# Performance work log

Hardware: AMD Instinct MI355X
Metric: run time of the kernel (lower is better)

## Reference

```python
import jax, jax.numpy as jnp
import numpy as np

# model dims
D = 2048      # hidden_size
H = 16        # num_attention_heads
KV = 4        # num_key_value_heads
DH = 128      # head_dim
RD = 64       # rotary_dim (partial RoPE)
E = 8         # num_local_experts
TOPK = 2      # num_experts_per_tok
I = 1024      # intermediate_size
EPS = 1e-6
THETA = 1000000.0


def rmsnorm(h, w, eps=EPS):
    dt = h.dtype
    h32 = h.astype(jnp.float32)
    var = jnp.mean(h32 * h32, axis=-1, keepdims=True)
    return (w * (h32 * jax.lax.rsqrt(var + eps))).astype(dt)


def rotate_half(t):
    half = t.shape[-1] // 2
    return jnp.concatenate([-t[..., half:], t[..., :half]], axis=-1)


def setup_inputs() -> dict:
    key = jax.random.key(0)
    ks = jax.random.split(key, 16)
    s = lambda k, shape, sc: (jax.random.normal(k, shape, dtype=jnp.float32) * sc)
    B, S = 1, 2048
    return {
        "x": s(ks[0], (B, S, D), 1.0),
        "ln1_w": jnp.ones((D,), jnp.float32),
        "ln2_w": jnp.ones((D,), jnp.float32),
        "wq": s(ks[1], (D, H * DH), 0.02),
        "wk": s(ks[2], (D, KV * DH), 0.02),
        "wv": s(ks[3], (D, KV * DH), 0.02),
        "wo": s(ks[4], (H * DH, D), 0.02),
        "qnorm_w": jnp.ones((H * DH,), jnp.float32),
        "knorm_w": jnp.ones((KV * DH,), jnp.float32),
        "router_w": s(ks[5], (D, E), 0.02),
        "router_bias": s(ks[6], (E,), 0.1),
        "wg": s(ks[7], (E, D, I), 0.02),
        "wu": s(ks[8], (E, D, I), 0.02),
        "wd": s(ks[9], (E, I, D), 0.02),
    }


def reference(x, ln1_w, ln2_w, wq, wk, wv, wo, qnorm_w, knorm_w,
              router_w, router_bias, wg, wu, wd):
    B, S, _ = x.shape
    # ---- input RMSNorm + attention ----
    res = x
    h = rmsnorm(x, ln1_w)
    q = h @ wq                           # [B,S,H*DH]
    k = h @ wk                           # [B,S,KV*DH]
    v = h @ wv
    # MiniMax M2: QK-norm BEFORE reshape, over the full projection dim
    q = rmsnorm(q, qnorm_w)
    k = rmsnorm(k, knorm_w)
    q = q.reshape(B, S, H, DH).transpose(0, 2, 1, 3)    # [B,H,S,DH]
    k = k.reshape(B, S, KV, DH).transpose(0, 2, 1, 3)   # [B,KV,S,DH]
    v = v.reshape(B, S, KV, DH).transpose(0, 2, 1, 3)
    # partial RoPE on first RD dims of each head
    pos = jnp.arange(S, dtype=jnp.float32)
    inv_freq = 1.0 / (THETA ** (jnp.arange(0, RD, 2, dtype=jnp.float32) / RD))
    ang = pos[:, None] * inv_freq[None, :]              # [S,RD/2]
    emb = jnp.concatenate([ang, ang], axis=-1)          # [S,RD]
    cos, sin = jnp.cos(emb), jnp.sin(emb)

    def rope(t):
        rot, pas = t[..., :RD], t[..., RD:]
        rot = rot * cos + rotate_half(rot) * sin
        return jnp.concatenate([rot, pas], axis=-1)

    q, k = rope(q), rope(k)
    # GQA: repeat kv heads
    rep = H // KV
    k = jnp.repeat(k, rep, axis=1)                      # [B,H,S,DH]
    v = jnp.repeat(v, rep, axis=1)
    scores = jnp.einsum("bhqd,bhkd->bhqk", q, k) / np.sqrt(DH)
    causal = jnp.tril(jnp.ones((S, S), dtype=bool))
    scores = jnp.where(causal, scores, jnp.finfo(jnp.float32).min)
    attn = jax.nn.softmax(scores.astype(jnp.float32), axis=-1).astype(q.dtype)
    o = jnp.einsum("bhqk,bhkd->bhqd", attn, v)          # [B,H,S,DH]
    o = o.transpose(0, 2, 1, 3).reshape(B, S, H * DH) @ wo
    x1 = res + o

    # ---- post-attn RMSNorm + sigmoid-router top-k MoE ----
    h2 = rmsnorm(x1, ln2_w)
    t = h2.reshape(-1, D)                               # [T,D]
    T = t.shape[0]
    logits = t.astype(jnp.float32) @ router_w           # router in fp32
    sig = jax.nn.sigmoid(logits)                        # act before topk
    # bias only influences expert choice, not affinities
    _, topi = jax.lax.top_k(sig + router_bias, TOPK)    # [T,TOPK]
    aff = jnp.take_along_axis(sig, topi, axis=-1)
    aff = aff / jnp.sum(aff, axis=-1, keepdims=True)    # normalize_top_k_affinities
    combine = jnp.zeros((T, E), jnp.float32).at[
        jnp.arange(T)[:, None], topi].set(aff)          # [T,E] sparse combine weights
    # GLU expert MLPs (dense over experts; combine zeros out unrouted)
    gate = jnp.einsum("td,edi->tei", t, wg)
    up = jnp.einsum("td,edi->tei", t, wu)
    act = jax.nn.silu(gate) * up                        # [T,E,I]
    moe = jnp.einsum("te,tei,eid->td", combine.astype(t.dtype), act, wd)
    return x1 + moe.reshape(B, S, D)
```

## Files before the change

### kernel.cpp

```cpp
#include <hip/hip_runtime.h>
#include <hip/hip_bf16.h>
#include <stdint.h>
#include <math.h>

typedef __bf16 bf16;
typedef __bf16 bf16x8 __attribute__((ext_vector_type(8)));
typedef __bf16 bf16x4 __attribute__((ext_vector_type(4)));
typedef float  f32x4  __attribute__((ext_vector_type(4)));

#define SD 2048
#define DM 2048
#define NH 16
#define NKV 4
#define DHD 128
#define NE 8
#define NNI 1024

constexpr size_t OF_WQKVT = 0;
constexpr size_t OF_WGUT  = OF_WQKVT + 12582912ull;
constexpr size_t OF_WDT   = OF_WGUT  + 67108864ull;
constexpr size_t OF_WOT   = OF_WDT   + 33554432ull;
constexpr size_t OF_H     = OF_WOT   + 8388608ull;
constexpr size_t OF_QKV   = OF_H     + 8388608ull;
constexpr size_t OF_QB    = OF_QKV   + 25165824ull;
constexpr size_t OF_KB    = OF_QB    + 8388608ull;
constexpr size_t OF_VTB   = OF_KB    + 2097152ull;
constexpr size_t OF_X1    = OF_VTB   + 2097152ull;
constexpr size_t WS_NEED  = OF_X1    + 16777216ull;
constexpr size_t OF_ACT  = OF_QKV;
constexpr size_t OF_TB   = OF_WOT;
constexpr size_t OF_OB   = OF_H;
constexpr size_t OF_CNT  = OF_KB;
constexpr size_t OF_BLKE = OF_KB + 256;
constexpr size_t OF_BLKR = OF_KB + 512;
constexpr size_t OF_TOT  = OF_KB + 768;
constexpr size_t OF_TOPI = OF_KB + 1024;
constexpr size_t OF_TOPW = OF_KB + 16384;
constexpr size_t OF_IDXL = OF_KB + 65536;
constexpr size_t OF_WLST = OF_KB + 131072;
constexpr size_t OF_TMP0 = OF_H;
constexpr size_t OF_TMP1 = OF_WOT;

__device__ __forceinline__ void async16(void* lds, const void* g) {
  uint32_t lo = (uint32_t)(uintptr_t)lds;
  __builtin_amdgcn_global_load_lds(
      (const __attribute__((address_space(1))) uint32_t*)(uintptr_t)g,
      (__attribute__((address_space(3))) uint32_t*)lo,
      16, 0, 0);
}

__global__ void transpose_cvt(const float* __restrict__ in, int ild, long long inb,
                              bf16* __restrict__ out, int old_, long long outb,
                              int ost, int oroff)
{
  __shared__ float tile[32][33];
  const float* ip = in + (long long)blockIdx.z * inb;
  bf16* op = out + (long long)blockIdx.z * outb;
  int r0 = blockIdx.y * 32, c0 = blockIdx.x * 32;
  int tx = threadIdx.x, ty = threadIdx.y;
#pragma unroll
  for (int i = 0; i < 4; i++)
    tile[ty + i*8][tx] = ip[(size_t)(r0 + ty + i*8)*ild + c0 + tx];
  __syncthreads();
#pragma unroll
  for (int i = 0; i < 4; i++) {
    int cl = ty + i*8;
    op[(size_t)((c0 + cl)*ost + oroff)*old_ + r0 + tx] = (bf16)tile[tx][cl];
  }
}

__global__ __launch_bounds__(256)
void rmsnorm_k(const float* __restrict__ in, const float* __restrict__ w, bf16* __restrict__ outb)
{
  __shared__ float red[4];
  int s = blockIdx.x, t = threadIdx.x;
  const float* ip = in + (size_t)s * DM;
  float v[8]; float ss = 0.f;
#pragma unroll
  for (int i = 0; i < 8; i++) { v[i] = ip[t + i*256]; ss += v[i]*v[i]; }
#pragma unroll
  for (int off = 32; off > 0; off >>= 1) ss += __shfl_xor(ss, off);
  if ((t & 63) == 0) red[t >> 6] = ss;
  __syncthreads();
  float rn = rsqrtf((red[0]+red[1]+red[2]+red[3]) * (1.f/DM) + 1e-6f);
  bf16* op = outb + (size_t)s * DM;
#pragma unroll
  for (int i = 0; i < 8; i++) op[t + i*256] = (bf16)(v[i]*rn*w[t + i*256]);
}

__global__ __launch_bounds__(256)
void qrope_k(const float* __restrict__ qkv, const float* __restrict__ w, bf16* __restrict__ qout)
{
  __shared__ float row[2048];
  __shared__ float red[4];
  int s = blockIdx.x, t = threadIdx.x;
  const float* ip = qkv + (size_t)s * 3072;
  float ss = 0.f;
#pragma unroll
  for (int i = 0; i < 8; i++) { float x = ip[t + i*256]; row[t + i*256] = x; ss += x*x; }
#pragma unroll
  for (int off = 32; off > 0; off >>= 1) ss += __shfl_xor(ss, off);
  if ((t & 63) == 0) red[t >> 6] = ss;
  __syncthreads();
  float rn = rsqrtf((red[0]+red[1]+red[2]+red[3]) * (1.f/2048.f) + 1e-6f);
  const float sc = 0.08838834764831845f;
#pragma unroll
  for (int i = 0; i < 8; i++) {
    int idx = t + i*256;
    int d = idx & 127;
    float val = row[idx]*rn*w[idx];
    float o;
    if (d < 64) {
      int fi = d & 31;
      float ang = (float)s * expf(-(float)fi * (13.815510557964274f/32.f));
      float c, sn; sincosf(ang, &sn, &c);
      float pv = row[idx ^ 32]*rn*w[idx ^ 32];
      o = (d < 32) ? (val*c - pv*sn) : (val*c + pv*sn);
    } else o = val;
    qout[((size_t)(idx >> 7)*SD + s)*DHD + d] = (bf16)(o * sc);
  }
}

__global__ __launch_bounds__(128)
void krope_k(const float* __restrict__ qkv, const float* __restrict__ w, bf16* __restrict__ kout)
{
  __shared__ float row[512];
  __shared__ float red[2];
  int s = blockIdx.x, t = threadIdx.x;
  const float* ip = qkv + (size_t)s * 3072 + 2048;
  float ss = 0.f;
#pragma unroll
  for (int i = 0; i < 4; i++) { float x = ip[t + i*128]; row[t + i*128] = x; ss += x*x; }
#pragma unroll
  for (int off = 32; off > 0; off >>= 1) ss += __shfl_xor(ss, off);
  if ((t & 63) == 0) red[t >> 6] = ss;
  __syncthreads();
  float rn = rsqrtf((red[0]+red[1]) * (1.f/512.f) + 1e-6f);
#pragma unroll
  for (int i = 0; i < 4; i++) {
    int idx = t + i*128;
    int d = idx & 127;
    float val = row[idx]*rn*w[idx];
    float o;
    if (d < 64) {
      int fi = d & 31;
      float ang = (float)s * expf(-(float)fi * (13.815510557964274f/32.f));
      float c, sn; sincosf(ang, &sn, &c);
      float pv = row[idx ^ 32]*rn*w[idx ^ 32];
      o = (d < 32) ? (val*c - pv*sn) : (val*c + pv*sn);
    } else o = val;
    kout[((size_t)(idx >> 7)*SD + s)*DHD + d] = (bf16)o;
  }
}

template<int EPI>
__global__ __launch_bounds__(256)
void gemm_bt(const bf16* __restrict__ Ag, const bf16* __restrict__ Bg,
             float* __restrict__ Cg, const float* __restrict__ res,
             int M, int N, int K)
{
  __shared__ __align__(16) bf16 As[2][128*32];
  __shared__ __align__(16) bf16 Bs[2][128*32];
  const int tid = threadIdx.x;
  const int wv = tid >> 6, l = tid & 63;
  const int wm = wv >> 1, wn = wv & 1;
  const int bm = blockIdx.y * 128, bn = blockIdx.x * 128;
  const bf16* A  = Ag;
  const bf16* BT = Bg;

  f32x4 acc[4][4];
  const f32x4 vz = {0.f, 0.f, 0.f, 0.f};
#pragma unroll
  for (int i = 0; i < 4; i++)
#pragma unroll
    for (int j = 0; j < 4; j++) acc[i][j] = vz;

  auto stage = [&](int kt, int b) {
    int k0 = kt * 32;
#pragma unroll
    for (int c = 0; c < 2; c++) {
      int chunk = wv*2 + c;
      int row = chunk*16 + (l >> 2);
      int kc = (l & 3) * 8;
      async16(&As[b][chunk*512], A  + (size_t)(bm + row)*K + k0 + kc);
      async16(&Bs[b][chunk*512], BT + (size_t)(bn + row)*K + k0 + kc);
    }
  };

  int nkt = K >> 5;
  stage(0, 0);
  int buf = 0;
  for (int kt = 0; kt < nkt; ++kt) {
    __syncthreads();
    if (kt + 1 < nkt) stage(kt + 1, buf ^ 1);
    bf16x8 af[4], bfv[4];
#pragma unroll
    for (int m = 0; m < 4; m++)
      af[m] = *(const bf16x8*)&As[buf][(wm*64 + m*16 + (l & 15))*32 + (l >> 4)*8];
#pragma unroll
    for (int n = 0; n < 4; n++)
      bfv[n] = *(const bf16x8*)&Bs[buf][(wn*64 + n*16 + (l & 15))*32 + (l >> 4)*8];
#pragma unroll
    for (int m = 0; m < 4; m++)
#pragma unroll
      for (int n = 0; n < 4; n++)
        acc[m][n] = __builtin_amdgcn_mfma_f32_16x16x32_bf16(af[m], bfv[n], acc[m][n], 0, 0, 0);
    buf ^= 1;
  }

#pragma unroll
  for (int m = 0; m < 4; m++) {
#pragma unroll
    for (int n = 0; n < 4; n++) {
#pragma unroll
      for (int r = 0; r < 4; r++) {
        int row = bm + wm*64 + m*16 + (l >> 4)*4 + r;
        int col = bn + wn*64 + n*16 + (l & 15);
        float v = acc[m][n][r];
        if (EPI == 0) {
          Cg[(size_t)row*N + col] = v;
        } else {
          Cg[(size_t)row*N + col] = v + res[(size_t)row*N + col];
        }
      }
    }
  }
}

__global__ __launch_bounds__(256)
void gemm_moe_gu(const bf16* __restrict__ tb, const bf16* __restrict__ wgu,
                 bf16* __restrict__ act,
                 const int* __restrict__ cnt, const int* __restrict__ blk_e,
                 const int* __restrict__ blk_r0, const int* __restrict__ total_nblk,
                 const int* __restrict__ idxlist)
{
  const int by = blockIdx.y;
  if (by >= *total_nblk) return;
  const int e = blk_e[by], r0 = blk_r0[by], cn = cnt[e];
  __shared__ __align__(16) bf16 As[2][128*32];
  __shared__ __align__(16) bf16 Bs[2][128*32];
  const int tid = threadIdx.x;
  const int wv = tid >> 6, l = tid & 63;
  const int wm = wv >> 1, wn = wv & 1;
  const int bn = blockIdx.x * 128;
  const bf16* BT = wgu + (size_t)e*2048*2048;

  const bf16* Arow[2];
#pragma unroll
  for (int c = 0; c < 2; c++) {
    int chunk = wv*2 + c;
    int rp = r0 + chunk*16 + (l >> 2);
    int tok = (rp < cn) ? (idxlist[e*2048 + rp] & 0xFFFF) : 0;
    Arow[c] = tb + (size_t)tok*2048 + (l & 3)*8;
  }

  f32x4 acc[4][4];
  const f32x4 vz = {0.f, 0.f, 0.f, 0.f};
#pragma unroll
  for (int i = 0; i < 4; i++)
#pragma unroll
    for (int j = 0; j < 4; j++) acc[i][j] = vz;

  auto stage = [&](int kt, int b) {
    int k0 = kt * 32;
#pragma unroll
    for (int c = 0; c < 2; c++) {
      int chunk = wv*2 + c;
      int row = chunk*16 + (l >> 2);
      int kc = (l & 3) * 8;
      async16(&As[b][chunk*512], Arow[c] + k0);
      async16(&Bs[b][chunk*512], BT + (size_t)(bn + row)*2048 + k0 + kc);
    }
  };

  stage(0, 0);
  int buf = 0;
  for (int kt = 0; kt < 64; ++kt) {
    __syncthreads();
    if (kt + 1 < 64) stage(kt + 1, buf ^ 1);
    bf16x8 af[4], bfv[4];
#pragma unroll
    for (int m = 0; m < 4; m++)
      af[m] = *(const bf16x8*)&As[buf][(wm*64 + m*16 + (l & 15))*32 + (l >> 4)*8];
#pragma unroll
    for (int n = 0; n < 4; n++)
      bfv[n] = *(const bf16x8*)&Bs[buf][(wn*64 + n*16 + (l & 15))*32 + (l >> 4)*8];
#pragma unroll
    for (int m = 0; m < 4; m++)
#pragma unroll
      for (int n = 0; n < 4; n++)
        acc[m][n] = __builtin_amdgcn_mfma_f32_16x16x32_bf16(af[m], bfv[n], acc[m][n], 0, 0, 0);
    buf ^= 1;
  }

  bf16* ap = act + (size_t)e*2048*1024;
#pragma unroll
  for (int m = 0; m < 4; m++) {
#pragma unroll
    for (int n = 0; n < 4; n++) {
#pragma unroll
      for (int r = 0; r < 4; r++) {
        int lrow = wm*64 + m*16 + (l >> 4)*4 + r;
        int col = bn + wn*64 + n*16 + (l & 15);
        float v = acc[m][n][r];
        float p = __shfl_xor(v, 1);
        if (!(l & 1)) {
          float a = v / (1.f + __expf(-v)) * p;
          ap[(size_t)(r0 + lrow)*1024 + (col >> 1)] = (bf16)a;
        }
      }
    }
  }
}

__global__ __launch_bounds__(256)
void gemm_moe_dn(const bf16* __restrict__ act, const bf16* __restrict__ wdt,
                 bf16* __restrict__ tmp0, bf16* __restrict__ tmp1,
                 const int* __restrict__ cnt, const int* __restrict__ blk_e,
                 const int* __restrict__ blk_r0, const int* __restrict__ total_nblk,
                 const int* __restrict__ idxlist, const float* __restrict__ wlist)
{
  const int by = blockIdx.y;
  if (by >= *total_nblk) return;
  const int e = blk_e[by], r0 = blk_r0[by], cn = cnt[e];
  __shared__ __align__(16) bf16 As[2][128*32];
  __shared__ __align__(16) bf16 Bs[2][128*32];
  const int tid = threadIdx.x;
  const int wv = tid >> 6, l = tid & 63;
  const int wm = wv >> 1, wn = wv & 1;
  const int bn = blockIdx.x * 128;
  const bf16* A  = act + (size_t)e*2048*1024 + (size_t)r0*1024;
  const bf16* BT = wdt + (size_t)e*2048*1024;

  f32x4 acc[4][4];
  const f32x4 vz = {0.f, 0.f, 0.f, 0.f};
#pragma unroll
  for (int i = 0; i < 4; i++)
#pragma unroll
    for (int j = 0; j < 4; j++) acc[i][j] = vz;

  auto stage = [&](int kt, int b) {
    int k0 = kt * 32;
#pragma unroll
    for (int c = 0; c < 2; c++) {
      int chunk = wv*2 + c;
      int row = chunk*16 + (l >> 2);
      int kc = (l & 3) * 8;
      async16(&As[b][chunk*512], A  + (size_t)row*1024 + k0 + kc);
      async16(&Bs[b][chunk*512], BT + (size_t)(bn + row)*1024 + k0 + kc);
    }
  };

  stage(0, 0);
  int buf = 0;
  for (int kt = 0; kt < 32; ++kt) {
    __syncthreads();
    if (kt + 1 < 32) stage(kt + 1, buf ^ 1);
    bf16x8 af[4], bfv[4];
#pragma unroll
    for (int m = 0; m < 4; m++)
      af[m] = *(const bf16x8*)&As[buf][(wm*64 + m*16 + (l & 15))*32 + (l >> 4)*8];
#pragma unroll
    for (int n = 0; n < 4; n++)
      bfv[n] = *(const bf16x8*)&Bs[buf][(wn*64 + n*16 + (l & 15))*32 + (l >> 4)*8];
#pragma unroll
    for (int m = 0; m < 4; m++)
#pragma unroll
      for (int n = 0; n < 4; n++)
        acc[m][n] = __builtin_amdgcn_mfma_f32_16x16x32_bf16(af[m], bfv[n], acc[m][n], 0, 0, 0);
    buf ^= 1;
  }

#pragma unroll
  for (int m = 0; m < 4; m++) {
#pragma unroll
    for (int n = 0; n < 4; n++) {
#pragma unroll
      for (int r = 0; r < 4; r++) {
        int lrow = wm*64 + m*16 + (l >> 4)*4 + r;
        int rie = r0 + lrow;
        if (rie < cn) {
          int col = bn + wn*64 + n*16 + (l & 15);
          int pk = idxlist[e*2048 + rie];
          int t = pk & 0xFFFF, rank = pk >> 16;
          float w = wlist[e*2048 + rie];
          bf16* dst = rank ? tmp1 : tmp0;
          dst[(size_t)t*2048 + col] = (bf16)(w * acc[m][n][r]);
        }
      }
    }
  }
}

__global__ __launch_bounds__(256)
void router_k(const float* __restrict__ x1, const float* __restrict__ w2,
              const float* __restrict__ rw, const float* __restrict__ rb,
              int* __restrict__ top_i, float* __restrict__ top_w)
{
  int tok = blockIdx.x*4 + (threadIdx.x >> 6);
  int l = threadIdx.x & 63;
  const float* ip = x1 + (size_t)tok * DM;
  float tv[32]; float ss = 0.f;
#pragma unroll
  for (int i = 0; i < 32; i++) { float v = ip[l + i*64]; tv[i] = v; ss += v*v; }
#pragma unroll
  for (int off = 32; off > 0; off >>= 1) ss += __shfl_xor(ss, off);
  float rn = rsqrtf(ss * (1.f/DM) + 1e-6f);
  float acc[8];
#pragma unroll
  for (int e = 0; e < 8; e++) acc[e] = 0.f;
#pragma unroll
  for (int i = 0; i < 32; i++) {
    int d = l + i*64;
    float tval = tv[i]*rn*w2[d];
#pragma unroll
    for (int e = 0; e < 8; e++) acc[e] += tval * rw[d*8 + e];
  }
#pragma unroll
  for (int e = 0; e < 8; e++)
#pragma unroll
    for (int off = 32; off > 0; off >>= 1) acc[e] += __shfl_xor(acc[e], off);
  if (l == 0) {
    float sig[8], scv[8];
#pragma unroll
    for (int e = 0; e < 8; e++) { sig[e] = 1.f/(1.f + expf(-acc[e])); scv[e] = sig[e] + rb[e]; }
    int i0 = 0;
#pragma unroll
    for (int e = 1; e < 8; e++) if (scv[e] > scv[i0]) i0 = e;
    int i1 = (i0 == 0) ? 1 : 0;
#pragma unroll
    for (int e = 0; e < 8; e++) if (e != i0 && scv[e] > scv[i1]) i1 = e;
    float a0 = sig[i0], a1 = sig[i1], inv = 1.f/(a0 + a1);
    top_i[tok] = i0 | (i1 << 8);
    top_w[tok*2]   = a0*inv;
    top_w[tok*2+1] = a1*inv;
  }
}

__global__ __launch_bounds__(256)
void build_k(const int* __restrict__ top_i, const float* __restrict__ top_w,
             int* __restrict__ cnt, int* __restrict__ blk_e, int* __restrict__ blk_r0,
             int* __restrict__ total_nblk, int* __restrict__ idxlist, float* __restrict__ wlist)
{
  __shared__ int lcnt[8];
  int tid = threadIdx.x;
  if (tid < 8) lcnt[tid] = 0;
  __syncthreads();
  for (int t = tid; t < SD; t += 256) {
    int pk = top_i[t];
    int i0 = pk & 0xFF, i1 = (pk >> 8) & 0xFF;
    int p0 = atomicAdd(&lcnt[i0], 1);
    idxlist[i0*2048 + p0] = t;
    wlist [i0*2048 + p0] = top_w[t*2];
    int p1 = atomicAdd(&lcnt[i1], 1);
    idxlist[i1*2048 + p1] = t | (1 << 16);
    wlist [i1*2048 + p1] = top_w[t*2+1];
  }
  __syncthreads();
  if (tid < 8) cnt[tid] = lcnt[tid];
  if (tid == 0) {
    int tot = 0;
    for (int e = 0; e < 8; e++) {
      int nb = (lcnt[e] + 127) >> 7;
      for (int b = 0; b < nb; b++) { blk_e[tot] = e; blk_r0[tot] = b*128; tot++; }
    }
    *total_nblk = tot;
  }
}

__global__ __launch_bounds__(256)
void final_add(const float* __restrict__ x1, const bf16* __restrict__ t0,
               const bf16* __restrict__ t1, float* __restrict__ out)
{
  size_t i = ((size_t)blockIdx.x*256 + threadIdx.x) * 4;
  f32x4 a = *(const f32x4*)(x1 + i);
  bf16x4 b0 = *(const bf16x4*)(t0 + i);
  bf16x4 b1 = *(const bf16x4*)(t1 + i);
  f32x4 o;
#pragma unroll
  for (int j = 0; j < 4; j++) o[j] = a[j] + (float)b0[j] + (float)b1[j];
  *(f32x4*)(out + i) = o;
}

__global__ __launch_bounds__(256)
void flash(const bf16* __restrict__ qb, const bf16* __restrict__ kb,
           const bf16* __restrict__ vtb, bf16* __restrict__ ob)
{
  __shared__ __align__(16) bf16 Ks[64*128];
  __shared__ __align__(16) bf16 Vs[128*64];
  __shared__ __align__(16) bf16 Ps[4*16*64];
  const int tid = threadIdx.x, wv = tid >> 6, l = tid & 63;
  const int qt = blockIdx.x, h = blockIdx.y, g = h >> 2;

  const int qrow = qt*64 + wv*16 + (l & 15);
  bf16x8 qf[4];
#pragma unroll
  for (int f = 0; f < 4; f++)
    qf[f] = *(const bf16x8*)(qb + ((size_t)h*SD + qrow)*DHD + f*32 + (l >> 4)*8);

  float mrun[4], lrun[4];
#pragma unroll
  for (int r = 0; r < 4; r++) { mrun[r] = -1e30f; lrun[r] = 0.f; }
  f32x4 oac[8];
  const f32x4 vz = {0.f, 0.f, 0.f, 0.f};
#pragma unroll
  for (int d = 0; d < 8; d++) oac[d] = vz;

  for (int j = 0; j <= qt; ++j) {
#pragma unroll
    for (int c = 0; c < 4; c++) {
      int chunk = wv*4 + c;
      int rk = chunk*4 + (l >> 4);
      int ck = (l & 15) ^ (rk & 7);
      async16(&Ks[chunk*512], kb + ((size_t)g*SD + j*64 + rk)*DHD + ck*8);
      int rv = chunk*8 + (l >> 3);
      int cv = (l & 7) ^ (rv & 7);
      async16(&Vs[chunk*512], vtb + ((size_t)g*DHD + rv)*SD + j*64 + cv*8);
    }
    __syncthreads();

    f32x4 sf[4];
#pragma unroll
    for (int n = 0; n < 4; n++) sf[n] = vz;
#pragma unroll
    for (int f = 0; f < 4; f++) {
#pragma unroll
      for (int n = 0; n < 4; n++) {
        int row = n*16 + (l & 15);
        int cb = (f*64 + (l >> 4)*16) ^ ((row & 7) << 4);
        bf16x8 kf = *(const bf16x8*)((const char*)Ks + row*256 + cb);
        sf[n] = __builtin_amdgcn_mfma_f32_16x16x32_bf16(qf[f], kf, sf[n], 0, 0, 0);
      }
    }
    if (j == qt) {
#pragma unroll
      for (int n = 0; n < 4; n++)
#pragma unroll
        for (int r = 0; r < 4; r++) {
          int kvp = n*16 + (l & 15);
          int qp  = wv*16 + (l >> 4)*4 + r;
          if (kvp > qp) sf[n][r] = -1e30f;
        }
    }
#pragma unroll
    for (int r = 0; r < 4; r++) {
      float tm = fmaxf(fmaxf(sf[0][r], sf[1][r]), fmaxf(sf[2][r], sf[3][r]));
#pragma unroll
      for (int off = 8; off > 0; off >>= 1) tm = fmaxf(tm, __shfl_xor(tm, off));
      float mn = fmaxf(mrun[r], tm);
      float fac = __expf(mrun[r] - mn);
      mrun[r] = mn;
      float pe[4]; float ps = 0.f;
#pragma unroll
      for (int n = 0; n < 4; n++) { pe[n] = __expf(sf[n][r] - mn); ps += pe[n]; }
#pragma unroll
      for (int off = 8; off > 0; off >>= 1) ps += __shfl_xor(ps, off);
      lrun[r] = lrun[r]*fac + ps;
#pragma unroll
      for (int d = 0; d < 8; d++) oac[d][r] *= fac;
      int prow = (l >> 4)*4 + r;
#pragma unroll
      for (int n = 0; n < 4; n++) {
        int cbp = ((n*16 + (l & 15))*2) ^ ((prow & 7) << 4);
        *(bf16*)((char*)Ps + wv*2048 + prow*128 + cbp) = (bf16)pe[n];
      }
    }
#pragma unroll
    for (int ks = 0; ks < 2; ks++) {
      int pr = l & 15;
      int cbp = (ks*64 + (l >> 4)*16) ^ ((pr & 7) << 4);
      bf16x8 pa = *(const bf16x8*)((const char*)Ps + wv*2048 + pr*128 + cbp);
#pragma unroll
      for (int dt = 0; dt < 8; dt++) {
        int rv = dt*16 + (l & 15);
        int cbv = (ks*64 + (l >> 4)*16) ^ ((rv & 7) << 4);
        bf16x8 vf = *(const bf16x8*)((const char*)Vs + rv*128 + cbv);
        oac[dt] = __builtin_amdgcn_mfma_f32_16x16x32_bf16(pa, vf, oac[dt], 0, 0, 0);
      }
    }
    __syncthreads();
  }
#pragma unroll
  for (int dt = 0; dt < 8; dt++)
#pragma unroll
    for (int r = 0; r < 4; r++) {
      int s = qt*64 + wv*16 + (l >> 4)*4 + r;
      int d = dt*16 + (l & 15);
      ob[(size_t)s*DM + h*DHD + d] = (bf16)(oac[dt][r] / lrun[r]);
    }
}

extern "C" void kernel_launch(void* const* d_in, const int* in_sizes, int n_in,
                              void* d_out, int out_size, void* d_ws, size_t ws_size,
                              hipStream_t stream) {
  if (ws_size < WS_NEED) return;
  const float* x     = (const float*)d_in[0];
  const float* ln1_w = (const float*)d_in[1];
  const float* ln2_w = (const float*)d_in[2];
  const float* wq    = (const float*)d_in[3];
  const float* wk    = (const float*)d_in[4];
  const float* wv    = (const float*)d_in[5];
  const float* wo    = (const float*)d_in[6];
  const float* qnw   = (const float*)d_in[7];
  const float* knw   = (const float*)d_in[8];
  const float* rw    = (const float*)d_in[9];
  const float* rb    = (const float*)d_in[10];
  const float* wg    = (const float*)d_in[11];
  const float* wu    = (const float*)d_in[12];
  const float* wd    = (const float*)d_in[13];

  char* ws = (char*)d_ws;
  bf16*  wqkvT = (bf16*)(ws + OF_WQKVT);
  bf16*  wguT  = (bf16*)(ws + OF_WGUT);
  bf16*  wdT   = (bf16*)(ws + OF_WDT);
  bf16*  woT   = (bf16*)(ws + OF_WOT);
  bf16*  hb    = (bf16*)(ws + OF_H);
  float* qkvf  = (float*)(ws + OF_QKV);
  bf16*  qbb   = (bf16*)(ws + OF_QB);
  bf16*  kbb   = (bf16*)(ws + OF_KB);
  bf16*  vtbb  = (bf16*)(ws + OF_VTB);
  float* x1f   = (float*)(ws + OF_X1);
  bf16*  actb  = (bf16*)(ws + OF_ACT);
  bf16*  tbb   = (bf16*)(ws + OF_TB);
  bf16*  obb   = (bf16*)(ws + OF_OB);
  int*   cntp  = (int*)(ws + OF_CNT);
  int*   blke  = (int*)(ws + OF_BLKE);
  int*   blkr  = (int*)(ws + OF_BLKR);
  int*   totp  = (int*)(ws + OF_TOT);
  int*   topi  = (int*)(ws + OF_TOPI);
  float* topw  = (float*)(ws + OF_TOPW);
  int*   idxl  = (int*)(ws + OF_IDXL);
  float* wlst  = (float*)(ws + OF_WLST);
  bf16*  tmp0  = (bf16*)(ws + OF_TMP0);
  bf16*  tmp1  = (bf16*)(ws + OF_TMP1);
  float* outp  = (float*)d_out;

  dim3 b32(32, 8);
  transpose_cvt<<<dim3(64,64,1), b32, 0, stream>>>(wq, 2048, 0, wqkvT, 2048, 0, 1, 0);
  transpose_cvt<<<dim3(16,64,1), b32, 0, stream>>>(wk,  512, 0, wqkvT, 2048, 0, 1, 2048);
  transpose_cvt<<<dim3(16,64,1), b32, 0, stream>>>(wv,  512, 0, wqkvT, 2048, 0, 1, 2560);
  transpose_cvt<<<dim3(64,64,1), b32, 0, stream>>>(wo, 2048, 0, woT,   2048, 0, 1, 0);
  transpose_cvt<<<dim3(32,64,8), b32, 0, stream>>>(wg, 1024, 2048ll*1024, wguT, 2048, 2048ll*2048, 2, 0);
  transpose_cvt<<<dim3(32,64,8), b32, 0, stream>>>(wu, 1024, 2048ll*1024, wguT, 2048, 2048ll*2048, 2, 1);
  transpose_cvt<<<dim3(64,32,8), b32, 0, stream>>>(wd, 2048, 1024ll*2048, wdT,  1024, 2048ll*1024, 1, 0);

  rmsnorm_k<<<2048, 256, 0, stream>>>(x, ln1_w, hb);
  gemm_bt<0><<<dim3(24,16,1), 256, 0, stream>>>(hb, wqkvT, qkvf, nullptr, 2048, 3072, 2048);
  qrope_k<<<2048, 256, 0, stream>>>(qkvf, qnw, qbb);
  krope_k<<<2048, 128, 0, stream>>>(qkvf, knw, kbb);
  transpose_cvt<<<dim3(16,64,1), b32, 0, stream>>>(qkvf + 2560, 3072, 0, vtbb, 2048, 0, 1, 0);

  flash<<<dim3(32,16,1), 256, 0, stream>>>(qbb, kbb, vtbb, obb);

  gemm_bt<1><<<dim3(16,16,1), 256, 0, stream>>>(obb, woT, x1f, x, 2048, 2048, 2048);
  rmsnorm_k<<<2048, 256, 0, stream>>>(x1f, ln2_w, tbb);
  router_k<<<512, 256, 0, stream>>>(x1f, ln2_w, rw, rb, topi, topw);
  build_k<<<1, 256, 0, stream>>>(topi, topw, cntp, blke, blkr, totp, idxl, wlst);

  gemm_moe_gu<<<dim3(16,40,1), 256, 0, stream>>>(tbb, wguT, actb, cntp, blke, blkr, totp, idxl);
  gemm_moe_dn<<<dim3(16,40,1), 256, 0, stream>>>(actb, wdT, tmp0, tmp1, cntp, blke, blkr, totp, idxl, wlst);
  final_add<<<4096, 256, 0, stream>>>(x1f, tmp0, tmp1, outp);
}
```

Before: 630.4 us.

## Shrink GEMM M-tiles to 64, double-buffer flash KV, precompute RoPE table

```diff
diff --git a/kernel.cpp b/kernel.cpp
--- a/kernel.cpp
+++ b/kernel.cpp
@@ -30,11 +30,12 @@
 constexpr size_t OF_ACT  = OF_QKV;
 constexpr size_t OF_TB   = OF_WOT;
 constexpr size_t OF_OB   = OF_H;
+constexpr size_t OF_ROPET= OF_X1;
 constexpr size_t OF_CNT  = OF_KB;
-constexpr size_t OF_BLKE = OF_KB + 256;
-constexpr size_t OF_BLKR = OF_KB + 512;
-constexpr size_t OF_TOT  = OF_KB + 768;
-constexpr size_t OF_TOPI = OF_KB + 1024;
+constexpr size_t OF_BLKE = OF_KB + 512;
+constexpr size_t OF_BLKR = OF_KB + 1024;
+constexpr size_t OF_TOT  = OF_KB + 1536;
+constexpr size_t OF_TOPI = OF_KB + 2048;
 constexpr size_t OF_TOPW = OF_KB + 16384;
 constexpr size_t OF_IDXL = OF_KB + 65536;
 constexpr size_t OF_WLST = OF_KB + 131072;
@@ -70,6 +71,17 @@
 }
 
 __global__ __launch_bounds__(256)
+void rope_tab_k(float* __restrict__ tab)
+{
+  int i = blockIdx.x*256 + threadIdx.x;
+  int s = i >> 5, fi = i & 31;
+  float ang = (float)s * expf(-(float)fi * (13.815510557964274f/32.f));
+  float c, sn; sincosf(ang, &sn, &c);
+  tab[i*2]   = c;
+  tab[i*2+1] = sn;
+}
+
+__global__ __launch_bounds__(256)
 void rmsnorm_k(const float* __restrict__ in, const float* __restrict__ w, bf16* __restrict__ outb)
 {
   __shared__ float red[4];
@@ -89,12 +101,14 @@
 }
 
 __global__ __launch_bounds__(256)
-void qrope_k(const float* __restrict__ qkv, const float* __restrict__ w, bf16* __restrict__ qout)
+void qrope_k(const float* __restrict__ qkv, const float* __restrict__ w,
+             const float* __restrict__ tab, bf16* __restrict__ qout)
 {
   __shared__ float row[2048];
   __shared__ float red[4];
   int s = blockIdx.x, t = threadIdx.x;
   const float* ip = qkv + (size_t)s * 3072;
+  const float2* tab2 = (const float2*)tab;
   float ss = 0.f;
 #pragma unroll
   for (int i = 0; i < 8; i++) { float x = ip[t + i*256]; row[t + i*256] = x; ss += x*x; }
@@ -112,22 +126,23 @@
     float o;
     if (d < 64) {
       int fi = d & 31;
-      float ang = (float)s * expf(-(float)fi * (13.815510557964274f/32.f));
-      float c, sn; sincosf(ang, &sn, &c);
+      float2 cs = tab2[s*32 + fi];
       float pv = row[idx ^ 32]*rn*w[idx ^ 32];
-      o = (d < 32) ? (val*c - pv*sn) : (val*c + pv*sn);
+      o = (d < 32) ? (val*cs.x - pv*cs.y) : (val*cs.x + pv*cs.y);
     } else o = val;
     qout[((size_t)(idx >> 7)*SD + s)*DHD + d] = (bf16)(o * sc);
   }
 }
 
 __global__ __launch_bounds__(128)
-void krope_k(const float* __restrict__ qkv, const float* __restrict__ w, bf16* __restrict__ kout)
+void krope_k(const float* __restrict__ qkv, const float* __restrict__ w,
+             const float* __restrict__ tab, bf16* __restrict__ kout)
 {
   __shared__ float row[512];
   __shared__ float red[2];
   int s = blockIdx.x, t = threadIdx.x;
   const float* ip = qkv + (size_t)s * 3072 + 2048;
+  const float2* tab2 = (const float2*)tab;
   float ss = 0.f;
 #pragma unroll
   for (int i = 0; i < 4; i++) { float x = ip[t + i*128]; row[t + i*128] = x; ss += x*x; }
@@ -144,46 +159,51 @@
     float o;
     if (d < 64) {
       int fi = d & 31;
-      float ang = (float)s * expf(-(float)fi * (13.815510557964274f/32.f));
-      float c, sn; sincosf(ang, &sn, &c);
+      float2 cs = tab2[s*32 + fi];
       float pv = row[idx ^ 32]*rn*w[idx ^ 32];
-      o = (d < 32) ? (val*c - pv*sn) : (val*c + pv*sn);
+      o = (d < 32) ? (val*cs.x - pv*cs.y) : (val*cs.x + pv*cs.y);
     } else o = val;
     kout[((size_t)(idx >> 7)*SD + s)*DHD + d] = (bf16)o;
   }
 }
 
-template<int EPI>
+template<int EPI, int BM>
 __global__ __launch_bounds__(256)
 void gemm_bt(const bf16* __restrict__ Ag, const bf16* __restrict__ Bg,
              float* __restrict__ Cg, const float* __restrict__ res,
              int M, int N, int K)
 {
-  __shared__ __align__(16) bf16 As[2][128*32];
+  constexpr int WM  = BM/2;
+  constexpr int MI  = WM/16;
+  constexpr int NCH = (BM+128)/16;
+  constexpr int CPW = NCH/4;
+  __shared__ __align__(16) bf16 As[2][BM*32];
   __shared__ __align__(16) bf16 Bs[2][128*32];
   const int tid = threadIdx.x;
   const int wv = tid >> 6, l = tid & 63;
   const int wm = wv >> 1, wn = wv & 1;
-  const int bm = blockIdx.y * 128, bn = blockIdx.x * 128;
+  const int bm = blockIdx.y * BM, bn = blockIdx.x * 128;
   const bf16* A  = Ag;
   const bf16* BT = Bg;
 
-  f32x4 acc[4][4];
+  f32x4 acc[MI][4];
   const f32x4 vz = {0.f, 0.f, 0.f, 0.f};
 #pragma unroll
-  for (int i = 0; i < 4; i++)
+  for (int i = 0; i < MI; i++)
 #pragma unroll
     for (int j = 0; j < 4; j++) acc[i][j] = vz;
 
   auto stage = [&](int kt, int b) {
     int k0 = kt * 32;
-#pragma unroll
-    for (int c = 0; c < 2; c++) {
-      int chunk = wv*2 + c;
+    int kc = (l & 3) * 8;
+#pragma unroll
+    for (int c = 0; c < CPW; c++) {
+      int chunk = wv*CPW + c;
       int row = chunk*16 + (l >> 2);
-      int kc = (l & 3) * 8;
-      async16(&As[b][chunk*512], A  + (size_t)(bm + row)*K + k0 + kc);
-      async16(&Bs[b][chunk*512], BT + (size_t)(bn + row)*K + k0 + kc);
+      if (chunk < BM/16)
+        async16(&As[b][chunk*512], A  + (size_t)(bm + row)*K + k0 + kc);
+      else
+        async16(&Bs[b][(chunk - BM/16)*512], BT + (size_t)(bn + row - BM)*K + k0 + kc);
     }
   };
 
@@ -193,15 +213,15 @@
   for (int kt = 0; kt < nkt; ++kt) {
     __syncthreads();
     if (kt + 1 < nkt) stage(kt + 1, buf ^ 1);
-    bf16x8 af[4], bfv[4];
-#pragma unroll
-    for (int m = 0; m < 4; m++)
-      af[m] = *(const bf16x8*)&As[buf][(wm*64 + m*16 + (l & 15))*32 + (l >> 4)*8];
+    bf16x8 af[MI], bfv[4];
+#pragma unroll
+    for (int m = 0; m < MI; m++)
+      af[m] = *(const bf16x8*)&As[buf][(wm*WM + m*16 + (l & 15))*32 + (l >> 4)*8];
 #pragma unroll
     for (int n = 0; n < 4; n++)
       bfv[n] = *(const bf16x8*)&Bs[buf][(wn*64 + n*16 + (l & 15))*32 + (l >> 4)*8];
 #pragma unroll
-    for (int m = 0; m < 4; m++)
+    for (int m = 0; m < MI; m++)
 #pragma unroll
       for (int n = 0; n < 4; n++)
         acc[m][n] = __builtin_amdgcn_mfma_f32_16x16x32_bf16(af[m], bfv[n], acc[m][n], 0, 0, 0);
@@ -209,12 +229,12 @@
   }
 
 #pragma unroll
-  for (int m = 0; m < 4; m++) {
+  for (int m = 0; m < MI; m++) {
 #pragma unroll
     for (int n = 0; n < 4; n++) {
 #pragma unroll
       for (int r = 0; r < 4; r++) {
-        int row = bm + wm*64 + m*16 + (l >> 4)*4 + r;
+        int row = bm + wm*WM + m*16 + (l >> 4)*4 + r;
         int col = bn + wn*64 + n*16 + (l & 15);
         float v = acc[m][n][r];
         if (EPI == 0) {
@@ -237,7 +257,7 @@
   const int by = blockIdx.y;
   if (by >= *total_nblk) return;
   const int e = blk_e[by], r0 = blk_r0[by], cn = cnt[e];
-  __shared__ __align__(16) bf16 As[2][128*32];
+  __shared__ __align__(16) bf16 As[2][64*32];
   __shared__ __align__(16) bf16 Bs[2][128*32];
   const int tid = threadIdx.x;
   const int wv = tid >> 6, l = tid & 63;
@@ -245,31 +265,37 @@
   const int bn = blockIdx.x * 128;
   const bf16* BT = wgu + (size_t)e*2048*2048;
 
-  const bf16* Arow[2];
-#pragma unroll
-  for (int c = 0; c < 2; c++) {
-    int chunk = wv*2 + c;
-    int rp = r0 + chunk*16 + (l >> 2);
-    int tok = (rp < cn) ? (idxlist[e*2048 + rp] & 0xFFFF) : 0;
-    Arow[c] = tb + (size_t)tok*2048 + (l & 3)*8;
-  }
-
-  f32x4 acc[4][4];
+  const bf16* Aptr[3];
+#pragma unroll
+  for (int c = 0; c < 3; c++) {
+    int chunk = wv*3 + c;
+    Aptr[c] = tb;
+    if (chunk < 4) {
+      int rp = r0 + chunk*16 + (l >> 2);
+      int tok = (rp < cn) ? (idxlist[e*2048 + rp] & 0xFFFF) : 0;
+      Aptr[c] = tb + (size_t)tok*2048 + (l & 3)*8;
+    }
+  }
+
+  f32x4 acc[2][4];
   const f32x4 vz = {0.f, 0.f, 0.f, 0.f};
 #pragma unroll
-  for (int i = 0; i < 4; i++)
+  for (int i = 0; i < 2; i++)
 #pragma unroll
     for (int j = 0; j < 4; j++) acc[i][j] = vz;
 
   auto stage = [&](int kt, int b) {
     int k0 = kt * 32;
-#pragma unroll
-    for (int c = 0; c < 2; c++) {
-      int chunk = wv*2 + c;
-      int row = chunk*16 + (l >> 2);
-      int kc = (l & 3) * 8;
-      async16(&As[b][chunk*512], Arow[c] + k0);
-      async16(&Bs[b][chunk*512], BT + (size_t)(bn + row)*2048 + k0 + kc);
+    int kc = (l & 3) * 8;
+#pragma unroll
+    for (int c = 0; c < 3; c++) {
+      int chunk = wv*3 + c;
+      if (chunk < 4)
+        async16(&As[b][chunk*512], Aptr[c] + k0);
+      else {
+        int row = chunk*16 + (l >> 2) - 64;
+        async16(&Bs[b][(chunk-4)*512], BT + (size_t)(bn + row)*2048 + k0 + kc);
+      }
     }
   };
 
@@ -278,15 +304,15 @@
   for (int kt = 0; kt < 64; ++kt) {
     __syncthreads();
     if (kt + 1 < 64) stage(kt + 1, buf ^ 1);
-    bf16x8 af[4], bfv[4];
-#pragma unroll
-    for (int m = 0; m < 4; m++)
-      af[m] = *(const bf16x8*)&As[buf][(wm*64 + m*16 + (l & 15))*32 + (l >> 4)*8];
+    bf16x8 af[2], bfv[4];
+#pragma unroll
+    for (int m = 0; m < 2; m++)
+      af[m] = *(const bf16x8*)&As[buf][(wm*32 + m*16 + (l & 15))*32 + (l >> 4)*8];
 #pragma unroll
     for (int n = 0; n < 4; n++)
       bfv[n] = *(const bf16x8*)&Bs[buf][(wn*64 + n*16 + (l & 15))*32 + (l >> 4)*8];
 #pragma unroll
-    for (int m = 0; m < 4; m++)
+    for (int m = 0; m < 2; m++)
 #pragma unroll
       for (int n = 0; n < 4; n++)
         acc[m][n] = __builtin_amdgcn_mfma_f32_16x16x32_bf16(af[m], bfv[n], acc[m][n], 0, 0, 0);
@@ -295,12 +321,12 @@
 
   bf16* ap = act + (size_t)e*2048*1024;
 #pragma unroll
-  for (int m = 0; m < 4; m++) {
+  for (int m = 0; m < 2; m++) {
 #pragma unroll
     for (int n = 0; n < 4; n++) {
 #pragma unroll
       for (int r = 0; r < 4; r++) {
-        int lrow = wm*64 + m*16 + (l >> 4)*4 + r;
+        int lrow = wm*32 + m*16 + (l >> 4)*4 + r;
         int col = bn + wn*64 + n*16 + (l & 15);
         float v = acc[m][n][r];
         float p = __shfl_xor(v, 1);
@@ -323,7 +349,7 @@
   const int by = blockIdx.y;
   if (by >= *total_nblk) return;
   const int e = blk_e[by], r0 = blk_r0[by], cn = cnt[e];
-  __shared__ __align__(16) bf16 As[2][128*32];
+  __shared__ __align__(16) bf16 As[2][64*32];
   __shared__ __align__(16) bf16 Bs[2][128*32];
   const int tid = threadIdx.x;
   const int wv = tid >> 6, l = tid & 63;
@@ -332,22 +358,24 @@
   const bf16* A  = act + (size_t)e*2048*1024 + (size_t)r0*1024;
   const bf16* BT = wdt + (size_t)e*2048*1024;
 
-  f32x4 acc[4][4];
+  f32x4 acc[2][4];
   const f32x4 vz = {0.f, 0.f, 0.f, 0.f};
 #pragma unroll
-  for (int i = 0; i < 4; i++)
+  for (int i = 0; i < 2; i++)
 #pragma unroll
     for (int j = 0; j < 4; j++) acc[i][j] = vz;
 
   auto stage = [&](int kt, int b) {
     int k0 = kt * 32;
-#pragma unroll
-    for (int c = 0; c < 2; c++) {
-      int chunk = wv*2 + c;
+    int kc = (l & 3) * 8;
+#pragma unroll
+    for (int c = 0; c < 3; c++) {
+      int chunk = wv*3 + c;
       int row = chunk*16 + (l >> 2);
-      int kc = (l & 3) * 8;
-      async16(&As[b][chunk*512], A  + (size_t)row*1024 + k0 + kc);
-      async16(&Bs[b][chunk*512], BT + (size_t)(bn + row)*1024 + k0 + kc);
+      if (chunk < 4)
+        async16(&As[b][chunk*512], A  + (size_t)row*1024 + k0 + kc);
+      else
+        async16(&Bs[b][(chunk-4)*512], BT + (size_t)(bn + row - 64)*1024 + k0 + kc);
     }
   };
 
@@ -356,15 +384,15 @@
   for (int kt = 0; kt < 32; ++kt) {
     __syncthreads();
     if (kt + 1 < 32) stage(kt + 1, buf ^ 1);
-    bf16x8 af[4], bfv[4];
-#pragma unroll
-    for (int m = 0; m < 4; m++)
-      af[m] = *(const bf16x8*)&As[buf][(wm*64 + m*16 + (l & 15))*32 + (l >> 4)*8];
+    bf16x8 af[2], bfv[4];
+#pragma unroll
+    for (int m = 0; m < 2; m++)
+      af[m] = *(const bf16x8*)&As[buf][(wm*32 + m*16 + (l & 15))*32 + (l >> 4)*8];
 #pragma unroll
     for (int n = 0; n < 4; n++)
       bfv[n] = *(const bf16x8*)&Bs[buf][(wn*64 + n*16 + (l & 15))*32 + (l >> 4)*8];
 #pragma unroll
-    for (int m = 0; m < 4; m++)
+    for (int m = 0; m < 2; m++)
 #pragma unroll
       for (int n = 0; n < 4; n++)
         acc[m][n] = __builtin_amdgcn_mfma_f32_16x16x32_bf16(af[m], bfv[n], acc[m][n], 0, 0, 0);
@@ -372,12 +400,12 @@
   }
 
 #pragma unroll
-  for (int m = 0; m < 4; m++) {
+  for (int m = 0; m < 2; m++) {
 #pragma unroll
     for (int n = 0; n < 4; n++) {
 #pragma unroll
       for (int r = 0; r < 4; r++) {
-        int lrow = wm*64 + m*16 + (l >> 4)*4 + r;
+        int lrow = wm*32 + m*16 + (l >> 4)*4 + r;
         int rie = r0 + lrow;
         if (rie < cn) {
           int col = bn + wn*64 + n*16 + (l & 15);
@@ -461,8 +489,8 @@
   if (tid == 0) {
     int tot = 0;
     for (int e = 0; e < 8; e++) {
-      int nb = (lcnt[e] + 127) >> 7;
-      for (int b = 0; b < nb; b++) { blk_e[tot] = e; blk_r0[tot] = b*128; tot++; }
+      int nb = (lcnt[e] + 63) >> 6;
+      for (int b = 0; b < nb; b++) { blk_e[tot] = e; blk_r0[tot] = b*64; tot++; }
     }
     *total_nblk = tot;
   }
@@ -486,11 +514,12 @@
 void flash(const bf16* __restrict__ qb, const bf16* __restrict__ kb,
            const bf16* __restrict__ vtb, bf16* __restrict__ ob)
 {
-  __shared__ __align__(16) bf16 Ks[64*128];
-  __shared__ __align__(16) bf16 Vs[128*64];
+  __shared__ __align__(16) bf16 Ks[2][64*128];
+  __shared__ __align__(16) bf16 Vs[2][128*64];
   __shared__ __align__(16) bf16 Ps[4*16*64];
   const int tid = threadIdx.x, wv = tid >> 6, l = tid & 63;
-  const int qt = blockIdx.x, h = blockIdx.y, g = h >> 2;
+  const int h = blockIdx.y, g = h >> 2;
+  const int qt = (h & 8) ? (31 - (int)blockIdx.x) : (int)blockIdx.x;
 
   const int qrow = qt*64 + wv*16 + (l & 15);
   bf16x8 qf[4];
@@ -506,32 +535,40 @@
 #pragma unroll
   for (int d = 0; d < 8; d++) oac[d] = vz;
 
-  for (int j = 0; j <= qt; ++j) {
+  auto stage = [&](int j, int b) {
 #pragma unroll
     for (int c = 0; c < 4; c++) {
       int chunk = wv*4 + c;
       int rk = chunk*4 + (l >> 4);
       int ck = (l & 15) ^ (rk & 7);
-      async16(&Ks[chunk*512], kb + ((size_t)g*SD + j*64 + rk)*DHD + ck*8);
+      async16(&Ks[b][chunk*512], kb + ((size_t)g*SD + j*64 + rk)*DHD + ck*8);
       int rv = chunk*8 + (l >> 3);
       int cv = (l & 7) ^ (rv & 7);
-      async16(&Vs[chunk*512], vtb + ((size_t)g*DHD + rv)*SD + j*64 + cv*8);
-    }
+      async16(&Vs[b][chunk*512], vtb + ((size_t)g*DHD + rv)*SD + j*64 + cv*8);
+    }
+  };
+
+  stage(0, 0);
+  int buf = 0;
+  for (int j = 0; j <= qt; ++j) {
     __syncthreads();
+    if (j < qt) stage(j + 1, buf ^ 1);
 
     f32x4 sf[4];
 #pragma unroll
     for (int n = 0; n < 4; n++) sf[n] = vz;
+    __builtin_amdgcn_s_setprio(1);
 #pragma unroll
     for (int f = 0; f < 4; f++) {
 #pragma unroll
       for (int n = 0; n < 4; n++) {
         int row = n*16 + (l & 15);
         int cb = (f*64 + (l >> 4)*16) ^ ((row & 7) << 4);
-        bf16x8 kf = *(const bf16x8*)((const char*)Ks + row*256 + cb);
+        bf16x8 kf = *(const bf16x8*)((const char*)Ks[buf] + row*256 + cb);
         sf[n] = __builtin_amdgcn_mfma_f32_16x16x32_bf16(qf[f], kf, sf[n], 0, 0, 0);
       }
     }
+    __builtin_amdgcn_s_setprio(0);
     if (j == qt) {
 #pragma unroll
       for (int n = 0; n < 4; n++)
@@ -565,6 +602,7 @@
         *(bf16*)((char*)Ps + wv*2048 + prow*128 + cbp) = (bf16)pe[n];
       }
     }
+    __builtin_amdgcn_s_setprio(1);
 #pragma unroll
     for (int ks = 0; ks < 2; ks++) {
       int pr = l & 15;
@@ -574,11 +612,12 @@
       for (int dt = 0; dt < 8; dt++) {
         int rv = dt*16 + (l & 15);
         int cbv = (ks*64 + (l >> 4)*16) ^ ((rv & 7) << 4);
-        bf16x8 vf = *(const bf16x8*)((const char*)Vs + rv*128 + cbv);
+        bf16x8 vf = *(const bf16x8*)((const char*)Vs[buf] + rv*128 + cbv);
         oac[dt] = __builtin_amdgcn_mfma_f32_16x16x32_bf16(pa, vf, oac[dt], 0, 0, 0);
       }
     }
-    __syncthreads();
+    __builtin_amdgcn_s_setprio(0);
+    buf ^= 1;
   }
 #pragma unroll
   for (int dt = 0; dt < 8; dt++)
@@ -620,6 +659,7 @@
   bf16*  kbb   = (bf16*)(ws + OF_KB);
   bf16*  vtbb  = (bf16*)(ws + OF_VTB);
   float* x1f   = (float*)(ws + OF_X1);
+  float* ropet = (float*)(ws + OF_ROPET);
   bf16*  actb  = (bf16*)(ws + OF_ACT);
   bf16*  tbb   = (bf16*)(ws + OF_TB);
   bf16*  obb   = (bf16*)(ws + OF_OB);
@@ -643,21 +683,22 @@
   transpose_cvt<<<dim3(32,64,8), b32, 0, stream>>>(wg, 1024, 2048ll*1024, wguT, 2048, 2048ll*2048, 2, 0);
   transpose_cvt<<<dim3(32,64,8), b32, 0, stream>>>(wu, 1024, 2048ll*1024, wguT, 2048, 2048ll*2048, 2, 1);
   transpose_cvt<<<dim3(64,32,8), b32, 0, stream>>>(wd, 2048, 1024ll*2048, wdT,  1024, 2048ll*1024, 1, 0);
+  rope_tab_k<<<256, 256, 0, stream>>>(ropet);
 
   rmsnorm_k<<<2048, 256, 0, stream>>>(x, ln1_w, hb);
-  gemm_bt<0><<<dim3(24,16,1), 256, 0, stream>>>(hb, wqkvT, qkvf, nullptr, 2048, 3072, 2048);
-  qrope_k<<<2048, 256, 0, stream>>>(qkvf, qnw, qbb);
-  krope_k<<<2048, 128, 0, stream>>>(qkvf, knw, kbb);
+  gemm_bt<0,64><<<dim3(24,32,1), 256, 0, stream>>>(hb, wqkvT, qkvf, nullptr, 2048, 3072, 2048);
+  qrope_k<<<2048, 256, 0, stream>>>(qkvf, qnw, ropet, qbb);
+  krope_k<<<2048, 128, 0, stream>>>(qkvf, knw, ropet, kbb);
   transpose_cvt<<<dim3(16,64,1), b32, 0, stream>>>(qkvf + 2560, 3072, 0, vtbb, 2048, 0, 1, 0);
 
   flash<<<dim3(32,16,1), 256, 0, stream>>>(qbb, kbb, vtbb, obb);
 
-  gemm_bt<1><<<dim3(16,16,1), 256, 0, stream>>>(obb, woT, x1f, x, 2048, 2048, 2048);
+  gemm_bt<1,64><<<dim3(16,32,1), 256, 0, stream>>>(obb, woT, x1f, x, 2048, 2048, 2048);
   rmsnorm_k<<<2048, 256, 0, stream>>>(x1f, ln2_w, tbb);
   router_k<<<512, 256, 0, stream>>>(x1f, ln2_w, rw, rb, topi, topw);
   build_k<<<1, 256, 0, stream>>>(topi, topw, cntp, blke, blkr, totp, idxl, wlst);
 
-  gemm_moe_gu<<<dim3(16,40,1), 256, 0, stream>>>(tbb, wguT, actb, cntp, blke, blkr, totp, idxl);
-  gemm_moe_dn<<<dim3(16,40,1), 256, 0, stream>>>(actb, wdT, tmp0, tmp1, cntp, blke, blkr, totp, idxl, wlst);
+  gemm_moe_gu<<<dim3(16,72,1), 256, 0, stream>>>(tbb, wguT, actb, cntp, blke, blkr, totp, idxl);
+  gemm_moe_dn<<<dim3(16,72,1), 256, 0, stream>>>(actb, wdT, tmp0, tmp1, cntp, blke, blkr, totp, idxl, wlst);
   final_add<<<4096, 256, 0, stream>>>(x1f, tmp0, tmp1, outp);
 }
```

After: 621.6 us. About the same (-1.4%).
